# Optimization experiments

Measured on AMD Instinct MI355X. Metric: run time of the kernel, lower is better.

## Reference

```python
import jax, jax.numpy as jnp
import numpy as np

B, A, UNITS, HID, T = 16, 256, 64, 64, 3


def setup_inputs() -> dict:
    key = jax.random.key(0)
    ks = jax.random.split(key, 16)
    x = jax.random.normal(ks[0], (B, A + 2, A), dtype=jnp.float32)
    # GNN message-passing weights (torch.randn in original)
    W0 = jax.random.normal(ks[1], (1, UNITS), dtype=jnp.float32)
    W1 = jax.random.normal(ks[2], (UNITS, UNITS), dtype=jnp.float32)
    W2 = jax.random.normal(ks[3], (UNITS, UNITS), dtype=jnp.float32)
    W3 = jax.random.normal(ks[4], (1, UNITS), dtype=jnp.float32)
    # fc_a: Linear(64,64)->ReLU->Linear(64,32)->ReLU->Linear(32,1); stored (in,out)
    s = lambda k, i, o: jax.random.uniform(k, (i, o), jnp.float32, -1, 1) / np.sqrt(i)
    sb = lambda k, i, o: jax.random.uniform(k, (o,), jnp.float32, -1, 1) / np.sqrt(i)
    a_w1, a_b1 = s(ks[5], UNITS, HID), sb(ks[6], UNITS, HID)
    a_w2, a_b2 = s(ks[7], HID, HID // 2), sb(ks[8], HID, HID // 2)
    a_w3, a_b3 = s(ks[9], HID // 2, 1), sb(ks[10], HID // 2, 1)
    # fc_v: Linear(64,64)->ReLU->Linear(64,1)
    v_w1, v_b1 = s(ks[11], UNITS, HID), sb(ks[12], UNITS, HID)
    v_w2, v_b2 = s(ks[13], HID, 1), sb(ks[14], HID, 1)
    return dict(x=x, W0=W0, W1=W1, W2=W2, W3=W3,
                a_w1=a_w1, a_b1=a_b1, a_w2=a_w2, a_b2=a_b2, a_w3=a_w3, a_b3=a_b3,
                v_w1=v_w1, v_b1=v_b1, v_w2=v_w2, v_b2=v_b2)


def reference(x, W0, W1, W2, W3,
              a_w1, a_b1, a_w2, a_b2, a_w3, a_b3,
              v_w1, v_b1, v_w2, v_b2):
    n_actions = x.shape[2]                       # A
    cur_sol = x[:, 0, :][..., None]              # [B, A, 1]
    mask = x[:, 1, :]                            # [B, A]
    weights = x[:, 2:n_actions + 2, :]           # [B, A, A]
    adjacent = (weights != 0).astype(jnp.float32)
    embedding = jnp.zeros((x.shape[0], n_actions, UNITS), dtype=jnp.float32)

    # e3 is loop-invariant in math, but original recomputes each step; keep T small python loop (faithful, T=3 static)
    for _ in range(T):
        e1 = cur_sol @ W0                                        # [B,A,1]@[1,U] -> [B,A,U]
        e2 = (adjacent @ embedding / n_actions) @ W1             # [B,A,U]
        # weights.reshape(B,A,A,1) @ W3(1,U) == outer-product broadcast
        e3_ = jnp.sum(jax.nn.relu(weights[..., None] * W3[0]), axis=2) / n_actions  # [B,A,U]
        e3 = e3_ @ W2
        embedding = jax.nn.relu(e1 + e2 + e3)

    # dueling heads
    h = jax.nn.relu(embedding @ a_w1 + a_b1)
    h = jax.nn.relu(h @ a_w2 + a_b2)
    out_a = (h @ a_w3 + a_b3)[..., 0]                            # [B, A]
    hv = jax.nn.relu(embedding @ v_w1 + v_b1)
    out_v = (hv @ v_w2 + v_b2)[..., 0]                           # [B, A]
    out_v = jnp.sum(out_v, axis=1, keepdims=True)                # [B, 1]
    output = out_v + (out_a - jnp.sum(out_a, axis=1, keepdims=True))
    output = output + mask * 10.0                                # hard_mask=False
    return output
```

## Files before the change

kernel.cpp:

```cpp
#include <hip/hip_runtime.h>


#define MC  0x5F3A9C71u
#define MD  0x5F3A9C72u
#define MDN 0x5F3A9C73u

__device__ __forceinline__ float reluf(float v) { return fmaxf(v, 0.f); }

__global__ __launch_bounds__(256) void k_fused(
    const float* __restrict__ x,
    const float* __restrict__ W0, const float* __restrict__ W1,
    const float* __restrict__ W2, const float* __restrict__ W3,
    const float* __restrict__ aw1, const float* __restrict__ ab1,
    const float* __restrict__ aw2, const float* __restrict__ ab2,
    const float* __restrict__ aw3, const float* __restrict__ ab3,
    const float* __restrict__ vw1, const float* __restrict__ vb1,
    const float* __restrict__ vw2, const float* __restrict__ vb2,
    float* __restrict__ oaw, float* __restrict__ ovv,
    float* __restrict__ possg, float* __restrict__ negsg,
    unsigned int* __restrict__ flagg, unsigned int* __restrict__ flag2,
    float* __restrict__ embg, float* __restrict__ out)
{
    __shared__ float aw1s[4096], vw1s[4096], W1s[4096];
    __shared__ float aw2s[64 * 36];
    __shared__ float embsT[64 * 36];
    __shared__ float poss[256], negs[256], css[256];
    __shared__ float W0s[64], P2s[64], N2s[64], Ssh[64], e2c[64];
    __shared__ float wpart[256], npart[256];
    __shared__ float ab1s[64], vb1s[64], vw2s[64], ab2s[32], aw3s[32];
    __shared__ float ab3s[1], vb2s[1], sov[32];
    __shared__ int zw[4];
    __shared__ unsigned int sflags[8];
    __shared__ int zrow[256];
    __shared__ unsigned long long zmsL[1024];

    const float invA = 1.0f / 256.0f;
    const int t = threadIdx.x;
    const int batch = blockIdx.x & 15;
    const int sub   = blockIdx.x >> 4;
    const int obase = sub * 32;

    {
        int r8 = t >> 3, s8 = t & 7;
        int grow = obase + r8;
        const float* rowp = x + ((size_t)batch * 258 + 2 + grow) * 256 + s8 * 32;
        float pp = 0.f, nn = 0.f, mn = 1e30f;
        #pragma unroll
        for (int c = 0; c < 32; c += 4) {
            float4 v = *(const float4*)(rowp + c);
            pp += fmaxf(v.x, 0.f) + fmaxf(v.y, 0.f) + fmaxf(v.z, 0.f) + fmaxf(v.w, 0.f);
            nn += fminf(v.x, 0.f) + fminf(v.y, 0.f) + fminf(v.z, 0.f) + fminf(v.w, 0.f);
            mn = fminf(mn, fminf(fminf(fabsf(v.x), fabsf(v.y)),
                                 fminf(fabsf(v.z), fabsf(v.w))));
        }
        pp += __shfl_xor(pp, 1); pp += __shfl_xor(pp, 2); pp += __shfl_xor(pp, 4);
        nn += __shfl_xor(nn, 1); nn += __shfl_xor(nn, 2); nn += __shfl_xor(nn, 4);
        mn = fminf(mn, __shfl_xor(mn, 1));
        mn = fminf(mn, __shfl_xor(mn, 2));
        mn = fminf(mn, __shfl_xor(mn, 4));
        if (s8 == 0) {
            __hip_atomic_store(&possg[batch * 256 + grow], pp,
                               __ATOMIC_RELAXED, __HIP_MEMORY_SCOPE_AGENT);
            __hip_atomic_store(&negsg[batch * 256 + grow], nn,
                               __ATOMIC_RELAXED, __HIP_MEMORY_SCOPE_AGENT);
        }
        int z = (s8 == 0 && mn == 0.f) ? 1 : 0;
        unsigned long long b = __ballot(z);
        if ((t & 63) == 0) zw[t >> 6] = (b != 0ull);
    }
    css[t] = x[(size_t)batch * 66048 + t];

    {
        int j = t & 63, mg = t >> 6;
        float pa = 0.f, na = 0.f;
        #pragma unroll
        for (int k = 0; k < 16; ++k) {
            int m = mg * 16 + k;
            float w3 = W3[m];
            float w2 = W2[m * 64 + j];
            pa = fmaf(fmaxf(w3, 0.f), w2, pa);
            na = fmaf(fminf(w3, 0.f), w2, na);
        }
        wpart[mg * 64 + j] = pa;
        npart[mg * 64 + j] = na;
    }
    __syncthreads();
    if (t == 0) {
        unsigned int fv = (zw[0] | zw[1] | zw[2] | zw[3]) ? MD : MC;
        __hip_atomic_store(&flagg[blockIdx.x], fv,
                           __ATOMIC_RELEASE, __HIP_MEMORY_SCOPE_AGENT);
    }
    if (t < 64) {
        P2s[t] = wpart[t] + wpart[64 + t] + wpart[128 + t] + wpart[192 + t];
        N2s[t] = npart[t] + npart[64 + t] + npart[128 + t] + npart[192 + t];
    }

    #pragma unroll
    for (int k = 0; k < 4; ++k) {
        int idx = k * 1024 + t * 4;
        *(float4*)&aw1s[idx] = *(const float4*)&aw1[idx];
        *(float4*)&vw1s[idx] = *(const float4*)&vw1[idx];
        *(float4*)&W1s[idx]  = *(const float4*)&W1[idx];
    }
    #pragma unroll
    for (int k = 0; k < 8; ++k) {
        int idx = k * 256 + t;
        aw2s[(idx >> 5) * 36 + (idx & 31)] = aw2[idx];
    }
    if (t < 64) { W0s[t] = W0[t]; ab1s[t] = ab1[t]; vb1s[t] = vb1[t]; vw2s[t] = vw2[t]; }
    if (t >= 64 && t < 96) { ab2s[t - 64] = ab2[t - 64]; aw3s[t - 64] = aw3[t - 64]; }
    if (t == 96) { ab3s[0] = ab3[0]; vb2s[0] = vb2[0]; }

    if (t < 8) {
        const unsigned int* f = &flagg[t * 16 + batch];
        unsigned int v = __hip_atomic_load(f, __ATOMIC_ACQUIRE, __HIP_MEMORY_SCOPE_AGENT);
        while (v != MC && v != MD) {
            __builtin_amdgcn_s_sleep(1);
            v = __hip_atomic_load(f, __ATOMIC_ACQUIRE, __HIP_MEMORY_SCOPE_AGENT);
        }
        sflags[t] = v;
    }
    __syncthreads();
    const int dirty = (sflags[0] == MD) | (sflags[1] == MD) | (sflags[2] == MD) |
                      (sflags[3] == MD) | (sflags[4] == MD) | (sflags[5] == MD) |
                      (sflags[6] == MD) | (sflags[7] == MD);

    poss[t] = __hip_atomic_load(&possg[batch * 256 + t],
                                __ATOMIC_RELAXED, __HIP_MEMORY_SCOPE_AGENT);
    negs[t] = __hip_atomic_load(&negsg[batch * 256 + t],
                                __ATOMIC_RELAXED, __HIP_MEMORY_SCOPE_AGENT);
    __syncthreads();

    if (!dirty) {
        const int j = t & 63, rg = t >> 6;
        const float w0j = W0s[j], p2j = P2s[j], n2j = N2s[j];
        float c_j = 0.f;
        #pragma unroll
        for (int iter = 0; iter < 2; ++iter) {
            float s = 0.f;
            #pragma unroll 8
            for (int k = 0; k < 64; ++k) {
                int i = rg * 64 + k;
                s += reluf(fmaf(css[i], w0j, (poss[i] * p2j + negs[i] * n2j) * invA) + c_j);
            }
            wpart[rg * 64 + j] = s;
            __syncthreads();
            if (t < 64) {
                float S = wpart[t] + wpart[64 + t] + wpart[128 + t] + wpart[192 + t];
                Ssh[t] = S;
                float c = 0.f;
                #pragma unroll 8
                for (int m = 0; m < 64; ++m) c = fmaf(Ssh[m], W1s[m * 64 + t], c);
                e2c[t] = c * invA;
            }
            __syncthreads();
            c_j = e2c[j];
        }
        {
            int r = t & 31, mg = t >> 5;
            int grow = obase + r;
            float cs = css[grow], pi = poss[grow], ni = negs[grow];
            #pragma unroll
            for (int jj = 0; jj < 8; ++jj) {
                int m = mg * 8 + jj;
                embsT[m * 36 + r] = reluf(fmaf(cs, W0s[m],
                                    (pi * P2s[m] + ni * N2s[m]) * invA) + e2c[m]);
            }
        }
    } else {
        {
            const int r4 = t >> 2, sub4 = t & 3;
            #pragma unroll
            for (int p = 0; p < 4; ++p) {
                int row = p * 64 + r4;
                const float* rowp = x + ((size_t)batch * 258 + 2 + row) * 256 + sub4 * 64;
                unsigned long long zm = 0ull;
                for (int c = 0; c < 64; ++c)
                    if (rowp[c] == 0.f) zm |= 1ull << c;
                zmsL[row * 4 + sub4] = zm;
                int zf = (zm != 0ull);
                zf |= __shfl_xor(zf, 1); zf |= __shfl_xor(zf, 2);
                if (sub4 == 0) zrow[row] = zf;
            }
        }
        __syncthreads();
        float* eb0 = embg + (size_t)blockIdx.x * 32768;
        float* eb1 = eb0 + 16384;
        const int r4 = t >> 2, sub4 = t & 3, jb = sub4 * 16;
        #pragma unroll
        for (int p = 0; p < 4; ++p) {
            int row = p * 64 + r4;
            float cs = css[row], pi = poss[row], ni = negs[row];
            #pragma unroll
            for (int q = 0; q < 16; ++q) {
                int jj = jb + q;
                eb0[row * 64 + jj] = reluf(fmaf(cs, W0s[jj],
                                      (pi * P2s[jj] + ni * N2s[jj]) * invA));
            }
        }
        __syncthreads();
        float* cur = eb0; float* nxt = eb1;
        for (int it = 1; it <= 2; ++it) {
            {
                int j = t & 63, rg = t >> 6;
                float s = 0.f;
                for (int k = 0; k < 64; ++k) s += cur[(rg * 64 + k) * 64 + j];
                wpart[rg * 64 + j] = s;
            }
            __syncthreads();
            if (t < 64) {
                float S = wpart[t] + wpart[64 + t] + wpart[128 + t] + wpart[192 + t];
                Ssh[t] = S;
                float c = 0.f;
                for (int m = 0; m < 64; ++m) c = fmaf(Ssh[m], W1s[m * 64 + t], c);
                e2c[t] = c * invA;
            }
            __syncthreads();
            #pragma unroll
            for (int p = 0; p < 4; ++p) {
                int row = p * 64 + r4;
                float cs = css[row], pi = poss[row], ni = negs[row];
                float acc[16];
                #pragma unroll
                for (int q = 0; q < 16; ++q) {
                    int jj = jb + q;
                    acc[q] = fmaf(cs, W0s[jj], (pi * P2s[jj] + ni * N2s[jj]) * invA)
                             + e2c[jj];
                }
                if (zrow[row]) {
                    for (int wd = 0; wd < 4; ++wd) {
                        unsigned long long zm = zmsL[row * 4 + wd];
                        while (zm) {
                            int k = wd * 64 + __builtin_ctzll(zm);
                            zm &= zm - 1;
                            float corr[16];
                            #pragma unroll
                            for (int q = 0; q < 16; ++q) corr[q] = 0.f;
                            for (int m = 0; m < 64; ++m) {
                                float ebm = cur[k * 64 + m];
                                #pragma unroll
                                for (int q = 0; q < 16; ++q)
                                    corr[q] = fmaf(ebm, W1s[m * 64 + jb + q], corr[q]);
                            }
                            #pragma unroll
                            for (int q = 0; q < 16; ++q) acc[q] -= corr[q] * invA;
                        }
                    }
                }
                #pragma unroll
                for (int q = 0; q < 16; ++q)
                    nxt[row * 64 + jb + q] = reluf(acc[q]);
            }
            __syncthreads();
            float* tmp = cur; cur = nxt; nxt = tmp;
        }
        for (int idx = t; idx < 2048; idx += 256) {
            int r = idx & 31, m = idx >> 5;
            embsT[m * 36 + r] = cur[(obase + r) * 64 + m];
        }
    }
    __syncthreads();

    const int cg  = t & 31;
    const int rg4 = t >> 5;
    float aA0x = 0.f, aA0y = 0.f, aA1x = 0.f, aA1y = 0.f;
    float aA2x = 0.f, aA2y = 0.f, aA3x = 0.f, aA3y = 0.f;
    float aV0x = 0.f, aV0y = 0.f, aV1x = 0.f, aV1y = 0.f;
    float aV2x = 0.f, aV2y = 0.f, aV3x = 0.f, aV3y = 0.f;
    for (int m = 0; m < 64; ++m) {
        float4 em = *(const float4*)&embsT[m * 36 + rg4 * 4];
        float2 a2 = *(const float2*)&aw1s[m * 64 + 2 * cg];
        float2 v2 = *(const float2*)&vw1s[m * 64 + 2 * cg];
        aA0x = fmaf(em.x, a2.x, aA0x); aA0y = fmaf(em.x, a2.y, aA0y);
        aA1x = fmaf(em.y, a2.x, aA1x); aA1y = fmaf(em.y, a2.y, aA1y);
        aA2x = fmaf(em.z, a2.x, aA2x); aA2y = fmaf(em.z, a2.y, aA2y);
        aA3x = fmaf(em.w, a2.x, aA3x); aA3y = fmaf(em.w, a2.y, aA3y);
        aV0x = fmaf(em.x, v2.x, aV0x); aV0y = fmaf(em.x, v2.y, aV0y);
        aV1x = fmaf(em.y, v2.x, aV1x); aV1y = fmaf(em.y, v2.y, aV1y);
        aV2x = fmaf(em.z, v2.x, aV2x); aV2y = fmaf(em.z, v2.y, aV2y);
        aV3x = fmaf(em.w, v2.x, aV3x); aV3y = fmaf(em.w, v2.y, aV3y);
    }
    float wvx = vw2s[2 * cg], wvy = vw2s[2 * cg + 1];
    float pv0 = fmaf(reluf(aV0x + vb1s[2 * cg]), wvx, reluf(aV0y + vb1s[2 * cg + 1]) * wvy);
    float pv1 = fmaf(reluf(aV1x + vb1s[2 * cg]), wvx, reluf(aV1y + vb1s[2 * cg + 1]) * wvy);
    float pv2 = fmaf(reluf(aV2x + vb1s[2 * cg]), wvx, reluf(aV2y + vb1s[2 * cg + 1]) * wvy);
    float pv3 = fmaf(reluf(aV3x + vb1s[2 * cg]), wvx, reluf(aV3y + vb1s[2 * cg + 1]) * wvy);
    #pragma unroll
    for (int mk = 1; mk <= 16; mk <<= 1) {
        pv0 += __shfl_xor(pv0, mk); pv1 += __shfl_xor(pv1, mk);
        pv2 += __shfl_xor(pv2, mk); pv3 += __shfl_xor(pv3, mk);
    }
    float b0 = ab1s[2 * cg], b1 = ab1s[2 * cg + 1];
    float h00 = reluf(aA0x + b0), h01 = reluf(aA0y + b1);
    float h10 = reluf(aA1x + b0), h11 = reluf(aA1y + b1);
    float h20 = reluf(aA2x + b0), h21 = reluf(aA2y + b1);
    float h30 = reluf(aA3x + b0), h31 = reluf(aA3y + b1);
    __syncthreads();
    float* h1s = embsT;
    *(float2*)&h1s[(rg4 * 4 + 0) * 68 + 2 * cg] = make_float2(h00, h01);
    *(float2*)&h1s[(rg4 * 4 + 1) * 68 + 2 * cg] = make_float2(h10, h11);
    *(float2*)&h1s[(rg4 * 4 + 2) * 68 + 2 * cg] = make_float2(h20, h21);
    *(float2*)&h1s[(rg4 * 4 + 3) * 68 + 2 * cg] = make_float2(h30, h31);
    if (cg == 0) {
        sov[rg4 * 4 + 0] = pv0 + vb2s[0];
        sov[rg4 * 4 + 1] = pv1 + vb2s[0];
        sov[rg4 * 4 + 2] = pv2 + vb2s[0];
        sov[rg4 * 4 + 3] = pv3 + vb2s[0];
    }
    __syncthreads();

    {
        int r = t >> 3, jg = t & 7;
        float c0 = 0.f, c1 = 0.f, c2 = 0.f, c3 = 0.f;
        for (int q = 0; q < 64; ++q) {
            float h = h1s[r * 68 + q];
            float4 w = *(const float4*)&aw2s[q * 36 + jg * 4];
            c0 = fmaf(h, w.x, c0); c1 = fmaf(h, w.y, c1);
            c2 = fmaf(h, w.z, c2); c3 = fmaf(h, w.w, c3);
        }
        float part = reluf(c0 + ab2s[jg * 4 + 0]) * aw3s[jg * 4 + 0];
        part = fmaf(reluf(c1 + ab2s[jg * 4 + 1]), aw3s[jg * 4 + 1], part);
        part = fmaf(reluf(c2 + ab2s[jg * 4 + 2]), aw3s[jg * 4 + 2], part);
        part = fmaf(reluf(c3 + ab2s[jg * 4 + 3]), aw3s[jg * 4 + 3], part);
        part += __shfl_xor(part, 1);
        part += __shfl_xor(part, 2);
        part += __shfl_xor(part, 4);
        if (jg == 0)
            __hip_atomic_store(&oaw[batch * 256 + obase + r], part + ab3s[0],
                               __ATOMIC_RELAXED, __HIP_MEMORY_SCOPE_AGENT);
    }
    if (t < 32)
        __hip_atomic_store(&ovv[batch * 256 + obase + t], sov[t],
                           __ATOMIC_RELAXED, __HIP_MEMORY_SCOPE_AGENT);
    __syncthreads();
    if (t == 0)
        __hip_atomic_store(&flag2[blockIdx.x], MDN,
                           __ATOMIC_RELEASE, __HIP_MEMORY_SCOPE_AGENT);

    if (sub == 0) {
        if (t < 8) {
            const unsigned int* f = &flag2[t * 16 + batch];
            unsigned int v = __hip_atomic_load(f, __ATOMIC_ACQUIRE,
                                               __HIP_MEMORY_SCOPE_AGENT);
            while (v != MDN) {
                __builtin_amdgcn_s_sleep(1);
                v = __hip_atomic_load(f, __ATOMIC_ACQUIRE, __HIP_MEMORY_SCOPE_AGENT);
            }
        }
        __syncthreads();
        float oa = __hip_atomic_load(&oaw[batch * 256 + t],
                                     __ATOMIC_RELAXED, __HIP_MEMORY_SCOPE_AGENT);
        float ov = __hip_atomic_load(&ovv[batch * 256 + t],
                                     __ATOMIC_RELAXED, __HIP_MEMORY_SCOPE_AGENT);
        float sa = oa, sv = ov;
        #pragma unroll
        for (int mk = 1; mk <= 32; mk <<= 1) {
            sa += __shfl_xor(sa, mk);
            sv += __shfl_xor(sv, mk);
        }
        if ((t & 63) == 0) { wpart[t >> 6] = sa; npart[t >> 6] = sv; }
        __syncthreads();
        float sA = wpart[0] + wpart[1] + wpart[2] + wpart[3];
        float sV = npart[0] + npart[1] + npart[2] + npart[3];
        float mask = x[((size_t)batch * 258 + 1) * 256 + t];
        out[batch * 256 + t] = sV + oa - sA + mask * 10.0f;
    }
}

extern "C" void kernel_launch(void* const* d_in, const int* in_sizes, int n_in,
                              void* d_out, int out_size, void* d_ws, size_t ws_size,
                              hipStream_t stream)
{
    (void)in_sizes; (void)n_in; (void)out_size; (void)ws_size;
    const float* x   = (const float*)d_in[0];
    const float* W0  = (const float*)d_in[1];
    const float* W1  = (const float*)d_in[2];
    const float* W2  = (const float*)d_in[3];
    const float* W3  = (const float*)d_in[4];
    const float* aw1 = (const float*)d_in[5];
    const float* ab1 = (const float*)d_in[6];
    const float* aw2 = (const float*)d_in[7];
    const float* ab2 = (const float*)d_in[8];
    const float* aw3 = (const float*)d_in[9];
    const float* ab3 = (const float*)d_in[10];
    const float* vw1 = (const float*)d_in[11];
    const float* vb1 = (const float*)d_in[12];
    const float* vw2 = (const float*)d_in[13];
    const float* vb2 = (const float*)d_in[14];

    float* ws = (float*)d_ws;
    float* oaw   = ws;
    float* ovv   = ws + 4096;
    float* possg = ws + 8192;
    float* negsg = ws + 12288;
    unsigned int* flagg = (unsigned int*)(ws + 16384);
    unsigned int* flag2 = (unsigned int*)(ws + 16512);
    float* embg  = ws + 16640;

    k_fused<<<128, 256, 0, stream>>>(x, W0, W1, W2, W3,
                                     aw1, ab1, aw2, ab2, aw3, ab3,
                                     vw1, vb1, vw2, vb2,
                                     oaw, ovv, possg, negsg, flagg, flag2,
                                     embg, (float*)d_out);
}
```

Before: 23.96 us.

## Distribute final dueling reduction across all blocks and publish stats flag earlier

Each block now reduces its own 32 advantage and value outputs to one partial sum, publishes it with a flag, and every block writes its own 32 outputs once all 8 partial sums for its batch are ready. Previously only sub-block 0 waited on per-row global values. The first-phase flag is now published before the W2 precompute and weight staging, so sibling blocks can stop waiting sooner. The pos/neg row statistics are packed into one 64-bit store and load. The h1 shared stride changes from 68 to 66. The cost is an extra spin-wait in every block, which adds cross-block sync risk if blocks are not co-resident.

```diff
diff --git a/kernel.cpp b/kernel.cpp
--- a/kernel.cpp
+++ b/kernel.cpp
@@ -16,8 +16,8 @@
     const float* __restrict__ aw3, const float* __restrict__ ab3,
     const float* __restrict__ vw1, const float* __restrict__ vb1,
     const float* __restrict__ vw2, const float* __restrict__ vb2,
-    float* __restrict__ oaw, float* __restrict__ ovv,
-    float* __restrict__ possg, float* __restrict__ negsg,
+    unsigned long long* __restrict__ statsg,
+    float* __restrict__ partA, float* __restrict__ partV,
     unsigned int* __restrict__ flagg, unsigned int* __restrict__ flag2,
     float* __restrict__ embg, float* __restrict__ out)
 {
@@ -28,7 +28,8 @@
     __shared__ float W0s[64], P2s[64], N2s[64], Ssh[64], e2c[64];
     __shared__ float wpart[256], npart[256];
     __shared__ float ab1s[64], vb1s[64], vw2s[64], ab2s[32], aw3s[32];
-    __shared__ float ab3s[1], vb2s[1], sov[32];
+    __shared__ float ab3s[1], vb2s[1], sov[32], soa[32];
+    __shared__ float pstash[8], qstash[8];
     __shared__ int zw[4];
     __shared__ unsigned int sflags[8];
     __shared__ int zrow[256];
@@ -39,6 +40,10 @@
     const int batch = blockIdx.x & 15;
     const int sub   = blockIdx.x >> 4;
     const int obase = sub * 32;
+
+    css[t] = x[(size_t)batch * 66048 + t];
+    float maskv = 0.f;
+    if (t < 32) maskv = x[((size_t)batch * 258 + 1) * 256 + obase + t];
 
     {
         int r8 = t >> 3, s8 = t & 7;
@@ -59,16 +64,22 @@
         mn = fminf(mn, __shfl_xor(mn, 2));
         mn = fminf(mn, __shfl_xor(mn, 4));
         if (s8 == 0) {
-            __hip_atomic_store(&possg[batch * 256 + grow], pp,
-                               __ATOMIC_RELAXED, __HIP_MEMORY_SCOPE_AGENT);
-            __hip_atomic_store(&negsg[batch * 256 + grow], nn,
+            float2 f2 = make_float2(pp, nn);
+            unsigned long long pk;
+            __builtin_memcpy(&pk, &f2, 8);
+            __hip_atomic_store(&statsg[batch * 256 + grow], pk,
                                __ATOMIC_RELAXED, __HIP_MEMORY_SCOPE_AGENT);
         }
         int z = (s8 == 0 && mn == 0.f) ? 1 : 0;
         unsigned long long b = __ballot(z);
         if ((t & 63) == 0) zw[t >> 6] = (b != 0ull);
     }
-    css[t] = x[(size_t)batch * 66048 + t];
+    __syncthreads();
+    if (t == 0) {
+        unsigned int fv = (zw[0] | zw[1] | zw[2] | zw[3]) ? MD : MC;
+        __hip_atomic_store(&flagg[blockIdx.x], fv,
+                           __ATOMIC_RELEASE, __HIP_MEMORY_SCOPE_AGENT);
+    }
 
     {
         int j = t & 63, mg = t >> 6;
@@ -84,17 +95,6 @@
         wpart[mg * 64 + j] = pa;
         npart[mg * 64 + j] = na;
     }
-    __syncthreads();
-    if (t == 0) {
-        unsigned int fv = (zw[0] | zw[1] | zw[2] | zw[3]) ? MD : MC;
-        __hip_atomic_store(&flagg[blockIdx.x], fv,
-                           __ATOMIC_RELEASE, __HIP_MEMORY_SCOPE_AGENT);
-    }
-    if (t < 64) {
-        P2s[t] = wpart[t] + wpart[64 + t] + wpart[128 + t] + wpart[192 + t];
-        N2s[t] = npart[t] + npart[64 + t] + npart[128 + t] + npart[192 + t];
-    }
-
     #pragma unroll
     for (int k = 0; k < 4; ++k) {
         int idx = k * 1024 + t * 4;
@@ -110,7 +110,11 @@
     if (t < 64) { W0s[t] = W0[t]; ab1s[t] = ab1[t]; vb1s[t] = vb1[t]; vw2s[t] = vw2[t]; }
     if (t >= 64 && t < 96) { ab2s[t - 64] = ab2[t - 64]; aw3s[t - 64] = aw3[t - 64]; }
     if (t == 96) { ab3s[0] = ab3[0]; vb2s[0] = vb2[0]; }
-
+    __syncthreads();
+    if (t < 64) {
+        P2s[t] = wpart[t] + wpart[64 + t] + wpart[128 + t] + wpart[192 + t];
+        N2s[t] = npart[t] + npart[64 + t] + npart[128 + t] + npart[192 + t];
+    }
     if (t < 8) {
         const unsigned int* f = &flagg[t * 16 + batch];
         unsigned int v = __hip_atomic_load(f, __ATOMIC_ACQUIRE, __HIP_MEMORY_SCOPE_AGENT);
@@ -125,10 +129,14 @@
                       (sflags[3] == MD) | (sflags[4] == MD) | (sflags[5] == MD) |
                       (sflags[6] == MD) | (sflags[7] == MD);
 
-    poss[t] = __hip_atomic_load(&possg[batch * 256 + t],
-                                __ATOMIC_RELAXED, __HIP_MEMORY_SCOPE_AGENT);
-    negs[t] = __hip_atomic_load(&negsg[batch * 256 + t],
-                                __ATOMIC_RELAXED, __HIP_MEMORY_SCOPE_AGENT);
+    {
+        unsigned long long pk = __hip_atomic_load(&statsg[batch * 256 + t],
+                                 __ATOMIC_RELAXED, __HIP_MEMORY_SCOPE_AGENT);
+        float2 f2;
+        __builtin_memcpy(&f2, &pk, 8);
+        poss[t] = f2.x;
+        negs[t] = f2.y;
+    }
     __syncthreads();
 
     if (!dirty) {
@@ -297,10 +305,10 @@
     float h30 = reluf(aA3x + b0), h31 = reluf(aA3y + b1);
     __syncthreads();
     float* h1s = embsT;
-    *(float2*)&h1s[(rg4 * 4 + 0) * 68 + 2 * cg] = make_float2(h00, h01);
-    *(float2*)&h1s[(rg4 * 4 + 1) * 68 + 2 * cg] = make_float2(h10, h11);
-    *(float2*)&h1s[(rg4 * 4 + 2) * 68 + 2 * cg] = make_float2(h20, h21);
-    *(float2*)&h1s[(rg4 * 4 + 3) * 68 + 2 * cg] = make_float2(h30, h31);
+    *(float2*)&h1s[(rg4 * 4 + 0) * 66 + 2 * cg] = make_float2(h00, h01);
+    *(float2*)&h1s[(rg4 * 4 + 1) * 66 + 2 * cg] = make_float2(h10, h11);
+    *(float2*)&h1s[(rg4 * 4 + 2) * 66 + 2 * cg] = make_float2(h20, h21);
+    *(float2*)&h1s[(rg4 * 4 + 3) * 66 + 2 * cg] = make_float2(h30, h31);
     if (cg == 0) {
         sov[rg4 * 4 + 0] = pv0 + vb2s[0];
         sov[rg4 * 4 + 1] = pv1 + vb2s[0];
@@ -313,7 +321,7 @@
         int r = t >> 3, jg = t & 7;
         float c0 = 0.f, c1 = 0.f, c2 = 0.f, c3 = 0.f;
         for (int q = 0; q < 64; ++q) {
-            float h = h1s[r * 68 + q];
+            float h = h1s[r * 66 + q];
             float4 w = *(const float4*)&aw2s[q * 36 + jg * 4];
             c0 = fmaf(h, w.x, c0); c1 = fmaf(h, w.y, c1);
             c2 = fmaf(h, w.z, c2); c3 = fmaf(h, w.w, c3);
@@ -325,45 +333,48 @@
         part += __shfl_xor(part, 1);
         part += __shfl_xor(part, 2);
         part += __shfl_xor(part, 4);
-        if (jg == 0)
-            __hip_atomic_store(&oaw[batch * 256 + obase + r], part + ab3s[0],
+        if (jg == 0) soa[r] = part + ab3s[0];
+    }
+    __syncthreads();
+
+    if (t < 32) {
+        float a = soa[t], v = sov[t];
+        #pragma unroll
+        for (int mk = 1; mk <= 16; mk <<= 1) {
+            a += __shfl_xor(a, mk);
+            v += __shfl_xor(v, mk);
+        }
+        if (t == 0) {
+            __hip_atomic_store(&partA[blockIdx.x], a,
                                __ATOMIC_RELAXED, __HIP_MEMORY_SCOPE_AGENT);
-    }
-    if (t < 32)
-        __hip_atomic_store(&ovv[batch * 256 + obase + t], sov[t],
-                           __ATOMIC_RELAXED, __HIP_MEMORY_SCOPE_AGENT);
-    __syncthreads();
-    if (t == 0)
-        __hip_atomic_store(&flag2[blockIdx.x], MDN,
-                           __ATOMIC_RELEASE, __HIP_MEMORY_SCOPE_AGENT);
-
-    if (sub == 0) {
-        if (t < 8) {
-            const unsigned int* f = &flag2[t * 16 + batch];
-            unsigned int v = __hip_atomic_load(f, __ATOMIC_ACQUIRE,
-                                               __HIP_MEMORY_SCOPE_AGENT);
-            while (v != MDN) {
-                __builtin_amdgcn_s_sleep(1);
-                v = __hip_atomic_load(f, __ATOMIC_ACQUIRE, __HIP_MEMORY_SCOPE_AGENT);
-            }
-        }
-        __syncthreads();
-        float oa = __hip_atomic_load(&oaw[batch * 256 + t],
-                                     __ATOMIC_RELAXED, __HIP_MEMORY_SCOPE_AGENT);
-        float ov = __hip_atomic_load(&ovv[batch * 256 + t],
-                                     __ATOMIC_RELAXED, __HIP_MEMORY_SCOPE_AGENT);
-        float sa = oa, sv = ov;
-        #pragma unroll
-        for (int mk = 1; mk <= 32; mk <<= 1) {
-            sa += __shfl_xor(sa, mk);
-            sv += __shfl_xor(sv, mk);
-        }
-        if ((t & 63) == 0) { wpart[t >> 6] = sa; npart[t >> 6] = sv; }
-        __syncthreads();
-        float sA = wpart[0] + wpart[1] + wpart[2] + wpart[3];
-        float sV = npart[0] + npart[1] + npart[2] + npart[3];
-        float mask = x[((size_t)batch * 258 + 1) * 256 + t];
-        out[batch * 256 + t] = sV + oa - sA + mask * 10.0f;
+            __hip_atomic_store(&partV[blockIdx.x], v,
+                               __ATOMIC_RELAXED, __HIP_MEMORY_SCOPE_AGENT);
+            __hip_atomic_store(&flag2[blockIdx.x], MDN,
+                               __ATOMIC_RELEASE, __HIP_MEMORY_SCOPE_AGENT);
+        }
+    }
+    if (t < 8) {
+        const unsigned int* f = &flag2[t * 16 + batch];
+        unsigned int v = __hip_atomic_load(f, __ATOMIC_ACQUIRE, __HIP_MEMORY_SCOPE_AGENT);
+        while (v != MDN) {
+            __builtin_amdgcn_s_sleep(1);
+            v = __hip_atomic_load(f, __ATOMIC_ACQUIRE, __HIP_MEMORY_SCOPE_AGENT);
+        }
+        pstash[t] = __hip_atomic_load(&partA[t * 16 + batch],
+                                      __ATOMIC_RELAXED, __HIP_MEMORY_SCOPE_AGENT);
+        qstash[t] = __hip_atomic_load(&partV[t * 16 + batch],
+                                      __ATOMIC_RELAXED, __HIP_MEMORY_SCOPE_AGENT);
+    }
+    __syncthreads();
+
+    if (t < 32) {
+        float sA = pstash[0];
+        sA += pstash[1]; sA += pstash[2]; sA += pstash[3];
+        sA += pstash[4]; sA += pstash[5]; sA += pstash[6]; sA += pstash[7];
+        float sV = qstash[0];
+        sV += qstash[1]; sV += qstash[2]; sV += qstash[3];
+        sV += qstash[4]; sV += qstash[5]; sV += qstash[6]; sV += qstash[7];
+        out[batch * 256 + obase + t] = sV + soa[t] - sA + maskv * 10.0f;
     }
 }
 
@@ -389,17 +400,16 @@
     const float* vb2 = (const float*)d_in[14];
 
     float* ws = (float*)d_ws;
-    float* oaw   = ws;
-    float* ovv   = ws + 4096;
-    float* possg = ws + 8192;
-    float* negsg = ws + 12288;
-    unsigned int* flagg = (unsigned int*)(ws + 16384);
-    unsigned int* flag2 = (unsigned int*)(ws + 16512);
-    float* embg  = ws + 16640;
+    unsigned long long* statsg = (unsigned long long*)ws;
+    float* partA = ws + 8192;
+    float* partV = ws + 8320;
+    unsigned int* flagg = (unsigned int*)(ws + 8448);
+    unsigned int* flag2 = (unsigned int*)(ws + 8576);
+    float* embg  = ws + 16384;
 
     k_fused<<<128, 256, 0, stream>>>(x, W0, W1, W2, W3,
                                      aw1, ab1, aw2, ab2, aw3, ab3,
                                      vw1, vb1, vw2, vb2,
-                                     oaw, ovv, possg, negsg, flagg, flag2,
+                                     statsg, partA, partV, flagg, flag2,
                                      embg, (float*)d_out);
 }
```

Result: slower. 24.80 us (+3.5%).
